# Optimization experiments

Measured on AMD Instinct MI355X. Metric: run time of the kernel, lower is better.

## Reference

```python
import jax, jax.numpy as jnp
import numpy as np

DIM = 64
HID = 128
DT_MAX = 0.1
BATCH = 16384


def _lin_init(k, fi, fo):
    kw, kb = jax.random.split(k)
    s = 1.0 / np.sqrt(fi)
    w = jax.random.uniform(kw, (fi, fo), minval=-s, maxval=s, dtype=jnp.float32)
    b = jax.random.uniform(kb, (fo,), minval=-s, maxval=s, dtype=jnp.float32)
    return w, b


def setup_inputs() -> dict:
    key = jax.random.key(0)
    ks = list(jax.random.split(key, 16))
    it = iter(ks)
    inp = {"z": jax.random.normal(next(it), (BATCH, DIM), dtype=jnp.float32)}
    layouts = [
        ("H", [(DIM, HID), (HID, HID), (HID, 1)]),
        ("D", [(DIM, HID), (HID, HID), (HID, 1)]),
        ("J", [(DIM, HID), (HID, DIM * DIM)]),
        ("B", [(DIM, HID), (HID, DIM * DIM)]),
        ("u", [(DIM, HID), (HID, DIM)]),
    ]
    for name, dims in layouts:
        for li, (fi, fo) in enumerate(dims, 1):
            w, b = _lin_init(next(it), fi, fo)
            inp[f"{name}w{li}"] = w
            inp[f"{name}b{li}"] = b
    inp["dt_logit"] = jnp.zeros((), dtype=jnp.float32)
    inp["energy_target"] = jnp.asarray(1.0, dtype=jnp.float32)
    return inp


def _scalar_net(z, w1, b1, w2, b2, w3, b3):
    # Linear->SiLU->Linear->SiLU->Linear, then softplus, squeeze -> [B]
    h = jax.nn.silu(z @ w1 + b1)
    h = jax.nn.silu(h @ w2 + b2)
    return jax.nn.softplus((h @ w3 + b3)[..., 0])


def reference(z, Hw1, Hb1, Hw2, Hb2, Hw3, Hb3,
              Dw1, Db1, Dw2, Db2, Dw3, Db3,
              Jw1, Jb1, Jw2, Jb2, Bw1, Bb1, Bw2, Bb2,
              uw1, ub1, uw2, ub2, dt_logit, energy_target):
    H = _scalar_net(z, Hw1, Hb1, Hw2, Hb2, Hw3, Hb3)  # [B]
    # autograd.grad(H.sum(), z) / grad(D.sum(), z)
    gH = jax.grad(lambda zz: _scalar_net(zz, Hw1, Hb1, Hw2, Hb2, Hw3, Hb3).sum())(z)
    gD = jax.grad(lambda zz: _scalar_net(zz, Dw1, Db1, Dw2, Db2, Dw3, Db3).sum())(z)
    # skew-symmetric J
    A = (jax.nn.silu(z @ Jw1 + Jb1) @ Jw2 + Jb2).reshape(-1, DIM, DIM)
    Jm = A - jnp.swapaxes(A, 1, 2)
    # PSD R = B B^T
    Bm = (jax.nn.silu(z @ Bw1 + Bb1) @ Bw2 + Bb2).reshape(-1, DIM, DIM)
    R = jnp.einsum('bik,bjk->bij', Bm, Bm)
    cons = jnp.einsum('bij,bj->bi', Jm, gH)
    diss = -jnp.einsum('bij,bj->bi', R, gD)
    u = jnp.tanh(z @ uw1 + ub1) @ uw2 + ub2
    pump = (energy_target - H)[:, None] * u
    dt = jax.nn.sigmoid(dt_logit) * DT_MAX
    dz = cons + diss + 0.1 * pump
    return z + dt * dz
```

## Files before the change

kernel.cpp:

```cpp
#include <hip/hip_runtime.h>

#define DIM 64
#define HID 128

typedef __attribute__((ext_vector_type(8))) short short8;
typedef __attribute__((ext_vector_type(4))) float f32x4;
typedef _Float16 h16x8 __attribute__((ext_vector_type(8)));
typedef _Float16 h16x2 __attribute__((ext_vector_type(2)));
typedef unsigned short ushort_t;

#define MFMA(A, B, C) __builtin_amdgcn_mfma_f32_16x16x32_bf16((A), (B), (C), 0, 0, 0)
#define MFMAH(A, B, C) __builtin_amdgcn_mfma_f32_16x16x32_f16((A), (B), (C), 0, 0, 0)
#define GLOAD_LDS(gp, lp) __builtin_amdgcn_global_load_lds( \
    (const __attribute__((address_space(1))) void*)(gp),    \
    (__attribute__((address_space(3))) void*)(lp), 16, 0, 0)

__device__ __forceinline__ float sigm(float x) { return 1.f / (1.f + __expf(-x)); }
__device__ __forceinline__ float siluf(float x) { return x * sigm(x); }
__device__ __forceinline__ float silup(float x) { float s = sigm(x); return s + x * s * (1.f - s); }
__device__ __forceinline__ float softplusf(float x) {
    if (x > 20.f) return x;
    return log1pf(__expf(x));
}
__device__ __forceinline__ ushort_t f2bf(float f) {
    union { float f; unsigned int u; } v; v.f = f;
    unsigned int r = v.u + 0x7fffu + ((v.u >> 16) & 1u);
    return (ushort_t)(r >> 16);
}
__device__ __forceinline__ ushort_t f2h(float f) {
    _Float16 h = (_Float16)f;
    union { _Float16 h; ushort_t u; } v; v.h = h; return v.u;
}
__device__ __forceinline__ _Float16 u2h(ushort_t u) {
    union { ushort_t u; _Float16 h; } v; v.u = u; return v.h;
}

#define OFF_HW1F  0
#define OFF_HW2F  8192
#define OFF_HW2TF 24576
#define OFF_HW1TF 40960
#define OFF_DW1F  49152
#define OFF_DW2F  57344
#define OFF_DW2TF 73728
#define OFF_DW1TF 90112
#define OFF_UW1F  98304
#define OFF_UW2F  106496
#define OFF_JW1F  114688
#define OFF_BW1F  122880

extern "C" __global__ __launch_bounds__(256)
void prep3_kernel(const float* __restrict__ Jw2, const float* __restrict__ Jb2,
                  const float* __restrict__ Bw2, const float* __restrict__ Bb2,
                  const float* __restrict__ Hw1, const float* __restrict__ Hw2,
                  const float* __restrict__ Dw1, const float* __restrict__ Dw2,
                  const float* __restrict__ uw1, const float* __restrict__ uw2,
                  const float* __restrict__ Jw1, const float* __restrict__ Bw1,
                  ushort_t* __restrict__ JW, ushort_t* __restrict__ BW1, ushort_t* __restrict__ BW2,
                  ushort_t* __restrict__ JbdF, ushort_t* __restrict__ Bb2F, ushort_t* __restrict__ Bb2TF,
                  ushort_t* __restrict__ SWF)
{
    const int b = blockIdx.x;
    if (b < 6144) {
        const int m = b >> 11;
        const int o = ((b & 2047) << 8) | threadIdx.x;
        const int e = o & 7, n = (o >> 3) & 63, g = (o >> 9) & 3, kt = o >> 11;
        const int k = (kt << 5) | (g << 3) | e;
        const int oi = k >> 7, h = k & 127;
        float val;
        if (m == 0)      val = Jw2[h * 4096 + n * 64 + oi] - Jw2[h * 4096 + oi * 64 + n];
        else if (m == 1) val = Bw2[h * 4096 + oi * 64 + n];
        else             val = Bw2[h * 4096 + n * 64 + oi];
        ushort_t* dst = (m == 0) ? JW : (m == 1) ? BW1 : BW2;
        dst[o] = f2h(val);
    } else if (b == 6144) {
        for (int e0 = threadIdx.x; e0 < 12288; e0 += 256) {
            const int m = e0 >> 12, o = e0 & 4095;
            const int e = o & 7, n = (o >> 3) & 63, g = (o >> 9) & 3, kb = o >> 11;
            const int k = (kb << 5) | (g << 3) | e;
            float val; ushort_t* dst;
            if (m == 0)      { val = Jb2[n * 64 + k] - Jb2[k * 64 + n]; dst = JbdF; }
            else if (m == 1) { val = Bb2[k * 64 + n];                   dst = Bb2F; }
            else             { val = Bb2[n * 64 + k];                   dst = Bb2TF; }
            dst[o] = f2h(val);
        }
    } else {
        const int e = (b - 6145) * 256 + threadIdx.x;
        float val = 0.f;
        if (e < 98304) {
            const int net = e / 49152;
            const int o = e - net * 49152;
            const float* W1s = net ? Dw1 : Hw1;
            const float* W2s = net ? Dw2 : Hw2;
            if (o < 8192) {
                int ks = o & 31, n = (o >> 5) & 127, kt = o >> 12;
                val = W1s[(kt * 32 + ks) * 128 + n];
            } else if (o < 24576) {
                int o2 = o - 8192;
                int ks = o2 & 31, n = (o2 >> 5) & 127, kt = o2 >> 12;
                val = W2s[(kt * 32 + ks) * 128 + n];
            } else if (o < 40960) {
                int o3 = o - 24576;
                int ks = o3 & 31, n = (o3 >> 5) & 127, kt = o3 >> 12;
                val = W2s[n * 128 + kt * 32 + ks];
            } else {
                int o4 = o - 40960;
                int ks = o4 & 31, n = (o4 >> 5) & 63, kt = o4 >> 11;
                val = W1s[n * 128 + kt * 32 + ks];
            }
        } else if (e < 106496) {
            int o = e - 98304;
            int ks = o & 31, n = (o >> 5) & 127, kt = o >> 12;
            val = uw1[(kt * 32 + ks) * 128 + n];
        } else if (e < 114688) {
            int o = e - 106496;
            int ks = o & 31, n = (o >> 5) & 63, kt = o >> 11;
            val = uw2[(kt * 32 + ks) * 64 + n];
        } else if (e < 122880) {
            int o = e - 114688;
            int ks = o & 31, n = (o >> 5) & 127, kt = o >> 12;
            val = Jw1[(kt * 32 + ks) * 128 + n];
        } else {
            int o = e - 122880;
            int ks = o & 31, n = (o >> 5) & 127, kt = o >> 12;
            val = Bw1[(kt * 32 + ks) * 128 + n];
        }
        SWF[e] = f2bf(val);
    }
}

__device__ __forceinline__ void scalar_net(
    int tid, int r0,
    const ushort_t* zbp, ushort_t* S1, ushort_t* S2, ushort_t* S3,
    float* yacc, float* srow, float* Hrow,
    const ushort_t* W1f, const ushort_t* W2f, const ushort_t* W2Tf, const ushort_t* W1Tf,
    const float* B1, const float* B2, const float* W3, const float* B3,
    ushort_t* gOut, int storeH)
{
    const int lane = tid & 63, w = tid >> 6;
    const int mt = w & 1, nh = w >> 1;
    const int cl = lane & 15, qq = lane >> 4;
    const int arow = mt * 16 + cl;
    const int crow = mt * 16 + qq * 4;

    {
        short8 a0 = *(const short8*)&zbp[arow * 72 + (qq << 3)];
        short8 a1 = *(const short8*)&zbp[arow * 72 + 32 + (qq << 3)];
        #pragma unroll
        for (int nt = 0; nt < 2; ++nt) {
            int n = nh * 32 + nt * 16 + cl;
            f32x4 acc = {0.f, 0.f, 0.f, 0.f};
            short8 b0 = *(const short8*)&W1f[(n << 5) + (qq << 3)];
            short8 b1 = *(const short8*)&W1f[((128 + n) << 5) + (qq << 3)];
            acc = MFMA(a0, b0, acc); acc = MFMA(a1, b1, acc);
            float bv = B1[n];
            #pragma unroll
            for (int q = 0; q < 4; ++q) {
                float aa = acc[q] + bv;
                S1[(crow + q) * 136 + n] = f2bf(siluf(aa));
                S2[(crow + q) * 136 + n] = f2bf(silup(aa));
            }
        }
    }
    __syncthreads();
    {
        short8 a[4];
        #pragma unroll
        for (int kt = 0; kt < 4; ++kt)
            a[kt] = *(const short8*)&S1[arow * 136 + kt * 32 + (qq << 3)];
        float yp[4] = {0.f, 0.f, 0.f, 0.f};
        #pragma unroll
        for (int nt = 0; nt < 2; ++nt) {
            int n = nh * 32 + nt * 16 + cl;
            f32x4 acc = {0.f, 0.f, 0.f, 0.f};
            #pragma unroll
            for (int kt = 0; kt < 4; ++kt) {
                short8 bb = *(const short8*)&W2f[((kt * 128 + n) << 5) + (qq << 3)];
                acc = MFMA(a[kt], bb, acc);
            }
            float bv = B2[n], w3v = W3[n];
            #pragma unroll
            for (int q = 0; q < 4; ++q) {
                float a2 = acc[q] + bv;
                yp[q] += siluf(a2) * w3v;
                S3[(crow + q) * 136 + n] = f2bf(w3v * silup(a2));
            }
        }
        #pragma unroll
        for (int q = 0; q < 4; ++q) {
            float p = yp[q];
            p += __shfl_xor(p, 1); p += __shfl_xor(p, 2);
            p += __shfl_xor(p, 4); p += __shfl_xor(p, 8);
            if (cl == 0) atomicAdd(&yacc[crow + q], p);
        }
    }
    __syncthreads();
    if (tid < 32) {
        float a3 = yacc[tid] + B3[0];
        srow[tid] = sigm(a3);
        if (storeH) Hrow[tid] = softplusf(a3);
        yacc[tid] = 0.f;
    }
    __syncthreads();
    {
        short8 a[4];
        #pragma unroll
        for (int kt = 0; kt < 4; ++kt)
            a[kt] = *(const short8*)&S3[arow * 136 + kt * 32 + (qq << 3)];
        #pragma unroll
        for (int nt = 0; nt < 2; ++nt) {
            int n = nh * 32 + nt * 16 + cl;
            f32x4 acc = {0.f, 0.f, 0.f, 0.f};
            #pragma unroll
            for (int kt = 0; kt < 4; ++kt) {
                short8 bb = *(const short8*)&W2Tf[((kt * 128 + n) << 5) + (qq << 3)];
                acc = MFMA(a[kt], bb, acc);
            }
            #pragma unroll
            for (int q = 0; q < 4; ++q) {
                float sp;
                { union { unsigned int u; float f; } v;
                  v.u = ((unsigned int)S2[(crow + q) * 136 + n]) << 16; sp = v.f; }
                S1[(crow + q) * 136 + n] = f2bf(acc[q] * sp);
            }
        }
    }
    __syncthreads();
    {
        short8 a[4];
        #pragma unroll
        for (int kt = 0; kt < 4; ++kt)
            a[kt] = *(const short8*)&S1[arow * 136 + kt * 32 + (qq << 3)];
        int n = nh * 16 + cl;
        f32x4 acc = {0.f, 0.f, 0.f, 0.f};
        #pragma unroll
        for (int kt = 0; kt < 4; ++kt) {
            short8 bb = *(const short8*)&W1Tf[((kt * 64 + n) << 5) + (qq << 3)];
            acc = MFMA(a[kt], bb, acc);
        }
        #pragma unroll
        for (int q = 0; q < 4; ++q) {
            int row = crow + q;
            gOut[(size_t)(r0 + row) * 64 + n] = f2h(srow[row] * acc[q]);
        }
    }
    __syncthreads();
}

extern "C" __global__ __launch_bounds__(512, 4)
void k1_kernel(const float* __restrict__ z,
               const float* __restrict__ Hb1, const float* __restrict__ Hb2,
               const float* __restrict__ Hw3, const float* __restrict__ Hb3,
               const float* __restrict__ Db1, const float* __restrict__ Db2,
               const float* __restrict__ Dw3, const float* __restrict__ Db3,
               const float* __restrict__ ub1, const float* __restrict__ ub2,
               const float* __restrict__ dtl, const float* __restrict__ etg,
               const ushort_t* __restrict__ SWF,
               ushort_t* __restrict__ gHbf, ushort_t* __restrict__ gDbf,
               float* __restrict__ out)
{
    __shared__ __align__(16) ushort_t zb[32][72];
    __shared__ __align__(16) ushort_t S1[32][136];
    __shared__ __align__(16) ushort_t S2[32][136];
    __shared__ __align__(16) ushort_t S3[32][136];
    __shared__ float yacc[32];
    __shared__ float srow[32];
    __shared__ float Hrow[32];

    const int tid = threadIdx.x;
    const int r0 = blockIdx.x * 32;

    {
        const float4* zg = (const float4*)(z + (size_t)r0 * 64);
        float4 v = zg[tid];
        int row = tid >> 4, c4 = (tid & 15) * 4;
        zb[row][c4 + 0] = f2bf(v.x); zb[row][c4 + 1] = f2bf(v.y);
        zb[row][c4 + 2] = f2bf(v.z); zb[row][c4 + 3] = f2bf(v.w);
        if (tid < 32) yacc[tid] = 0.f;
    }
    __syncthreads();

    scalar_net(tid, r0, &zb[0][0], &S1[0][0], &S2[0][0], &S3[0][0], yacc, srow, Hrow,
               SWF + OFF_HW1F, SWF + OFF_HW2F, SWF + OFF_HW2TF, SWF + OFF_HW1TF,
               Hb1, Hb2, Hw3, Hb3, gHbf, 1);
    scalar_net(tid, r0, &zb[0][0], &S1[0][0], &S2[0][0], &S3[0][0], yacc, srow, Hrow,
               SWF + OFF_DW1F, SWF + OFF_DW2F, SWF + OFF_DW2TF, SWF + OFF_DW1TF,
               Db1, Db2, Dw3, Db3, gDbf, 0);

    const int lane = tid & 63, w = tid >> 6;
    const int mt = w & 1, nh = w >> 1;
    const int cl = lane & 15, qq = lane >> 4;
    const int arow = mt * 16 + cl;
    const int crow = mt * 16 + qq * 4;

    {
        short8 a0 = *(const short8*)&zb[arow][(qq << 3)];
        short8 a1 = *(const short8*)&zb[arow][32 + (qq << 3)];
        const ushort_t* W1f = SWF + OFF_UW1F;
        #pragma unroll
        for (int nt = 0; nt < 2; ++nt) {
            int n = nh * 32 + nt * 16 + cl;
            f32x4 acc = {0.f, 0.f, 0.f, 0.f};
            short8 b0 = *(const short8*)&W1f[(n << 5) + (qq << 3)];
            short8 b1 = *(const short8*)&W1f[((128 + n) << 5) + (qq << 3)];
            acc = MFMA(a0, b0, acc); acc = MFMA(a1, b1, acc);
            float bv = ub1[n];
            #pragma unroll
            for (int q = 0; q < 4; ++q)
                S1[crow + q][n] = f2bf(tanhf(acc[q] + bv));
        }
    }
    __syncthreads();
    {
        short8 a[4];
        #pragma unroll
        for (int kt = 0; kt < 4; ++kt)
            a[kt] = *(const short8*)&S1[arow][kt * 32 + (qq << 3)];
        const ushort_t* W2f = SWF + OFF_UW2F;
        const float dtv = 0.1f * sigm(dtl[0]);
        const float et = etg[0];
        int n = nh * 16 + cl;
        f32x4 acc = {0.f, 0.f, 0.f, 0.f};
        #pragma unroll
        for (int kt = 0; kt < 4; ++kt) {
            short8 bb = *(const short8*)&W2f[((kt * 64 + n) << 5) + (qq << 3)];
            acc = MFMA(a[kt], bb, acc);
        }
        float bv = ub2[n];
        #pragma unroll
        for (int q = 0; q < 4; ++q) {
            int row = crow + q;
            size_t idx = (size_t)(r0 + row) * 64 + n;
            out[idx] = z[idx] + dtv * 0.1f * (et - Hrow[row]) * (acc[q] + bv);
        }
    }
}

#define LOADHF2H(SRC, HA, HB)                                                     \
    do {                                                                          \
        _Pragma("unroll")                                                         \
        for (int q4 = 0; q4 < 4; ++q4) {                                          \
            short8 sa = *(const short8*)&(SRC)[rr0][q4 * 32 + (qq << 3)];         \
            short8 sb = *(const short8*)&(SRC)[rr1][q4 * 32 + (qq << 3)];         \
            _Pragma("unroll")                                                     \
            for (int e = 0; e < 4; ++e) {                                         \
                h16x2 ta, tb;                                                     \
                ta[0] = u2h((ushort_t)sa[e * 2]); ta[1] = u2h((ushort_t)sa[e * 2 + 1]); \
                tb[0] = u2h((ushort_t)sb[e * 2]); tb[1] = u2h((ushort_t)sb[e * 2 + 1]); \
                (HA)[q4 * 4 + e] = ta;                                            \
                (HB)[q4 * 4 + e] = tb;                                            \
            }                                                                     \
        }                                                                         \
    } while (0)

#define STAGE(dst, src)                                                           \
    do {                                                                          \
        _Pragma("unroll")                                                         \
        for (int i_ = 0; i_ < 8; ++i_) {                                          \
            GLOAD_LDS((src) + ((w * 8 + i_) << 9) + (lane << 3),                  \
                      (dst) + ((w * 8 + i_) << 9));                               \
        }                                                                         \
    } while (0)

#define HEAVY_PASS(Wbase, BFbase, G, HA, HB, A00, A01, A10, A11)                  \
    do {                                                                          \
        STAGE(wst0, (Wbase));                                                     \
        __syncthreads();                                                          \
        _Pragma("unroll 1")                                                       \
        for (int t = 0; t < 32; ++t) {                                            \
            const ushort_t* curb = (t & 1) ? wst1 : wst0;                         \
            if (t < 31) STAGE((t & 1) ? wst0 : wst1, (Wbase) + (size_t)(t + 1) * 16384); \
            const int j = 2 * t + ks;                                             \
            _Float16 gA = u2h((G)[rr0][j]);                                       \
            _Float16 gB = u2h((G)[rr1][j]);                                       \
            h16x2 gA2; gA2[0] = gA; gA2[1] = gA;                                  \
            h16x2 gB2; gB2[0] = gB; gB2[1] = gB;                                  \
            _Pragma("unroll")                                                     \
            for (int ki = 0; ki < 4; ++ki) {                                      \
                const int tb = ((ks * 4 + ki) << 11) + (qq << 9);                 \
                h16x8 b0 = *(const h16x8*)&curb[tb + col0 * 8];                   \
                h16x8 b1 = *(const h16x8*)&curb[tb + col1 * 8];                   \
                union { h16x2 h2[4]; h16x8 v; } aA, aB;                           \
                _Pragma("unroll")                                                 \
                for (int e = 0; e < 4; ++e) {                                     \
                    aA.h2[e] = (HA)[ki * 4 + e] * gA2;                            \
                    aB.h2[e] = (HB)[ki * 4 + e] * gB2;                            \
                }                                                                 \
                A00 = MFMAH(aA.v, b0, A00); A01 = MFMAH(aA.v, b1, A01);           \
                A10 = MFMAH(aB.v, b0, A10); A11 = MFMAH(aB.v, b1, A11);           \
            }                                                                     \
            __syncthreads();                                                      \
        }                                                                         \
                             \
        {                                                                         \
            h16x8 abA = *(const h16x8*)&(G)[rr0][(ks << 5) + (qq << 3)];          \
            h16x8 abB = *(const h16x8*)&(G)[rr1][(ks << 5) + (qq << 3)];          \
            const ushort_t* bp = (BFbase) + (ks << 11) + (qq << 9);               \
            h16x8 b0 = *(const h16x8*)&bp[col0 * 8];                              \
            h16x8 b1 = *(const h16x8*)&bp[col1 * 8];                              \
            A00 = MFMAH(abA, b0, A00); A01 = MFMAH(abA, b1, A01);                 \
            A10 = MFMAH(abB, b0, A10); A11 = MFMAH(abB, b1, A11);                 \
        }                                                                         \
                                             \
        __syncthreads();                                                          \
        if (ks == 1) {                                                            \
            _Pragma("unroll")                                                     \
            for (int q = 0; q < 4; ++q) {                                         \
                Pb[orow0 + q][col0] = A00[q]; Pb[orow0 + q][col1] = A01[q];       \
                Pb[orow1 + q][col0] = A10[q]; Pb[orow1 + q][col1] = A11[q];       \
            }                                                                     \
        }                                                                         \
        __syncthreads();                                                          \
        if (ks == 0) {                                                            \
            _Pragma("unroll")                                                     \
            for (int q = 0; q < 4; ++q) {                                         \
                A00[q] += Pb[orow0 + q][col0]; A01[q] += Pb[orow0 + q][col1];     \
                A10[q] += Pb[orow1 + q][col0]; A11[q] += Pb[orow1 + q][col1];     \
            }                                                                     \
        }                                                                         \
        __syncthreads();                                                          \
    } while (0)

extern "C" __global__ __launch_bounds__(256, 2)
void k2_kernel(const float* __restrict__ z,
               const float* __restrict__ Jb1, const float* __restrict__ Bb1,
               const float* __restrict__ dtl,
               const ushort_t* __restrict__ JW, const ushort_t* __restrict__ BW1,
               const ushort_t* __restrict__ BW2,
               const ushort_t* __restrict__ JbdF, const ushort_t* __restrict__ Bb2F,
               const ushort_t* __restrict__ Bb2TF,
               const ushort_t* __restrict__ SWF,
               const ushort_t* __restrict__ gHbf, const ushort_t* __restrict__ gDbf,
               float* __restrict__ out)
{
    __shared__ __align__(16) ushort_t zb[32][72];
    __shared__ __align__(16) ushort_t hJ2[32][136];
    __shared__ __align__(16) ushort_t hB2[32][136];
    __shared__ __align__(16) ushort_t gHb[32][72];
    __shared__ __align__(16) ushort_t gDb[32][72];
    __shared__ __align__(16) ushort_t vb2[32][72];
    __shared__ __align__(16) float Pb[32][68];
    __shared__ __align__(16) ushort_t wst0[8192];
    __shared__ __align__(16) ushort_t wst1[8192];

    const int tid = threadIdx.x;
    const int r0 = blockIdx.x * 32;

    {
        const float4* zg = (const float4*)(z + (size_t)r0 * 64);
        #pragma unroll
        for (int it = 0; it < 2; ++it) {
            int i = it * 256 + tid;
            float4 v = zg[i];
            int row = i >> 4, c4 = (i & 15) * 4;
            zb[row][c4 + 0] = f2bf(v.x); zb[row][c4 + 1] = f2bf(v.y);
            zb[row][c4 + 2] = f2bf(v.z); zb[row][c4 + 3] = f2bf(v.w);
        }
        const short8* gh = (const short8*)(gHbf + (size_t)r0 * 64);
        const short8* gd = (const short8*)(gDbf + (size_t)r0 * 64);
        int row = tid >> 3, s = tid & 7;
        *(short8*)&gHb[row][s * 8] = gh[tid];
        *(short8*)&gDb[row][s * 8] = gd[tid];
    }
    __syncthreads();

    const int lane = tid & 63, w = tid >> 6;
    const int cl = lane & 15, qq = lane >> 4;
    const int mt = w & 1, nh = w >> 1;
    const int arow = mt * 16 + cl;
    const int crowL = mt * 16 + qq * 4;

    {
        short8 a0 = *(const short8*)&zb[arow][(qq << 3)];
        short8 a1 = *(const short8*)&zb[arow][32 + (qq << 3)];
        const ushort_t* JW1f = SWF + OFF_JW1F;
        const ushort_t* BW1f = SWF + OFF_BW1F;
        #pragma unroll
        for (int nt = 0; nt < 4; ++nt) {
            int n = nh * 64 + nt * 16 + cl;
            f32x4 accJ = {0.f, 0.f, 0.f, 0.f}, accB = {0.f, 0.f, 0.f, 0.f};
            short8 jb0 = *(const short8*)&JW1f[(n << 5) + (qq << 3)];
            short8 jb1 = *(const short8*)&JW1f[((128 + n) << 5) + (qq << 3)];
            accJ = MFMA(a0, jb0, accJ); accJ = MFMA(a1, jb1, accJ);
            short8 bb0 = *(const short8*)&BW1f[(n << 5) + (qq << 3)];
            short8 bb1 = *(const short8*)&BW1f[((128 + n) << 5) + (qq << 3)];
            accB = MFMA(a0, bb0, accB); accB = MFMA(a1, bb1, accB);
            float jbv = Jb1[n], bbv = Bb1[n];
            #pragma unroll
            for (int q = 0; q < 4; ++q) {
                hJ2[crowL + q][n] = f2h(siluf(accJ[q] + jbv));
                hB2[crowL + q][n] = f2h(siluf(accB[q] + bbv));
            }
        }
    }
    __syncthreads();

    const int ch = w & 1;
    const int ks = w >> 1;
    const int rr0 = cl;
    const int rr1 = cl + 16;
    const int col0 = ch * 32 + cl;
    const int col1 = col0 + 16;
    const int orow0 = qq * 4;
    const int orow1 = orow0 + 16;

    h16x2 hfJA[16], hfJB[16], hfBA[16], hfBB[16];
    f32x4 c00 = {0,0,0,0}, c01 = {0,0,0,0}, c10 = {0,0,0,0}, c11 = {0,0,0,0};
    f32x4 v00 = {0,0,0,0}, v01 = {0,0,0,0}, v10 = {0,0,0,0}, v11 = {0,0,0,0};
    f32x4 d00 = {0,0,0,0}, d01 = {0,0,0,0}, d10 = {0,0,0,0}, d11 = {0,0,0,0};

    LOADHF2H(hJ2, hfJA, hfJB);
    HEAVY_PASS(JW, JbdF, gHb, hfJA, hfJB, c00, c01, c10, c11);

    LOADHF2H(hB2, hfBA, hfBB);
    HEAVY_PASS(BW1, Bb2F, gDb, hfBA, hfBB, v00, v01, v10, v11);

    if (ks == 0) {
        #pragma unroll
        for (int q = 0; q < 4; ++q) {
            vb2[orow0 + q][col0] = f2h(v00[q]); vb2[orow0 + q][col1] = f2h(v01[q]);
            vb2[orow1 + q][col0] = f2h(v10[q]); vb2[orow1 + q][col1] = f2h(v11[q]);
        }
    }
    __syncthreads();

    HEAVY_PASS(BW2, Bb2TF, vb2, hfBA, hfBB, d00, d01, d10, d11);

    if (ks == 0) {
        const float dtv = 0.1f * sigm(dtl[0]);
        #pragma unroll
        for (int q = 0; q < 4; ++q) {
            size_t i00 = (size_t)(r0 + orow0 + q) * 64 + col0;
            size_t i01 = (size_t)(r0 + orow0 + q) * 64 + col1;
            size_t i10 = (size_t)(r0 + orow1 + q) * 64 + col0;
            size_t i11 = (size_t)(r0 + orow1 + q) * 64 + col1;
            out[i00] += dtv * (c00[q] - d00[q]);
            out[i01] += dtv * (c01[q] - d01[q]);
            out[i10] += dtv * (c10[q] - d10[q]);
            out[i11] += dtv * (c11[q] - d11[q]);
        }
    }
}

extern "C" void kernel_launch(void* const* d_in, const int* in_sizes, int n_in,
                              void* d_out, int out_size, void* d_ws, size_t ws_size,
                              hipStream_t stream) {
    const float* p[27];
    for (int i = 0; i < 27; ++i) p[i] = (const float*)d_in[i];
    ushort_t* JW    = (ushort_t*)d_ws;
    ushort_t* BW1   = JW + 524288;
    ushort_t* BW2   = BW1 + 524288;
    ushort_t* JbdF  = BW2 + 524288;
    ushort_t* Bb2F  = JbdF + 4096;
    ushort_t* Bb2TF = Bb2F + 4096;
    ushort_t* gHbf  = Bb2TF + 4096;
    ushort_t* gDbf  = gHbf + (size_t)16384 * 64;
    ushort_t* SWF   = gDbf + (size_t)16384 * 64;

    hipLaunchKernelGGL(prep3_kernel, dim3(6657), dim3(256), 0, stream,
                       p[15], p[16], p[19], p[20],
                       p[1], p[3], p[7], p[9],
                       p[21], p[23], p[13], p[17],
                       JW, BW1, BW2, JbdF, Bb2F, Bb2TF, SWF);

    const int batch = in_sizes[0] / DIM;
    hipLaunchKernelGGL(k1_kernel, dim3(batch / 32), dim3(512), 0, stream,
                       p[0],
                       p[2], p[4], p[5], p[6],
                       p[8], p[10], p[11], p[12],
                       p[22], p[24],
                       p[25], p[26],
                       SWF, gHbf, gDbf, (float*)d_out);

    hipLaunchKernelGGL(k2_kernel, dim3(batch / 32), dim3(256), 0, stream,
                       p[0], p[14], p[18], p[25],
                       JW, BW1, BW2, JbdF, Bb2F, Bb2TF, SWF,
                       gHbf, gDbf, (float*)d_out);
}
```

Baseline: 119.5 us.

## Load heavy-pass weight fragments directly from global memory instead of LDS staging

Replaces the double-buffered global-to-LDS staging of the large weight tiles in the heavy pass with direct per-lane global loads into registers, unrolled by two. This removes the per-iteration __syncthreads barriers and frees 32 KB of shared memory, which may allow more blocks per CU. In exchange, each wave fetches its weight fragments straight from global/L2 with no LDS-level sharing across waves, and load latency must be hidden by unrolling and occupancy.

New measurement: 112.5 us. -5.9%, faster.

```diff
diff --git a/kernel.cpp b/kernel.cpp
--- a/kernel.cpp
+++ b/kernel.cpp
@@ -11,9 +11,6 @@
 
 #define MFMA(A, B, C) __builtin_amdgcn_mfma_f32_16x16x32_bf16((A), (B), (C), 0, 0, 0)
 #define MFMAH(A, B, C) __builtin_amdgcn_mfma_f32_16x16x32_f16((A), (B), (C), 0, 0, 0)
-#define GLOAD_LDS(gp, lp) __builtin_amdgcn_global_load_lds( \
-    (const __attribute__((address_space(1))) void*)(gp),    \
-    (__attribute__((address_space(3))) void*)(lp), 16, 0, 0)
 
 __device__ __forceinline__ float sigm(float x) { return 1.f / (1.f + __expf(-x)); }
 __device__ __forceinline__ float siluf(float x) { return x * sigm(x); }
@@ -352,51 +349,41 @@
         }                                                                         \
     } while (0)
 
-#define STAGE(dst, src)                                                           \
-    do {                                                                          \
-        _Pragma("unroll")                                                         \
-        for (int i_ = 0; i_ < 8; ++i_) {                                          \
-            GLOAD_LDS((src) + ((w * 8 + i_) << 9) + (lane << 3),                  \
-                      (dst) + ((w * 8 + i_) << 9));                               \
-        }                                                                         \
-    } while (0)
-
 #define HEAVY_PASS(Wbase, BFbase, G, HA, HB, A00, A01, A10, A11)                  \
     do {                                                                          \
-        STAGE(wst0, (Wbase));                                                     \
-        __syncthreads();                                                          \
-        _Pragma("unroll 1")                                                       \
-        for (int t = 0; t < 32; ++t) {                                            \
-            const ushort_t* curb = (t & 1) ? wst1 : wst0;                         \
-            if (t < 31) STAGE((t & 1) ? wst0 : wst1, (Wbase) + (size_t)(t + 1) * 16384); \
-            const int j = 2 * t + ks;                                             \
+        _Pragma("unroll 2")                                                       \
+        for (int jj = 0; jj < 32; ++jj) {                                         \
+            const int j = 2 * jj + ks;                                            \
+            const ushort_t* bp = (Wbase) + (size_t)j * 8192 + (qq << 9);          \
+            h16x8 bf0[4], bf1[4];                                                 \
+            _Pragma("unroll")                                                     \
+            for (int ki = 0; ki < 4; ++ki) {                                      \
+                bf0[ki] = *(const h16x8*)&bp[ki * 2048 + col0 * 8];               \
+                bf1[ki] = *(const h16x8*)&bp[ki * 2048 + col1 * 8];               \
+            }                                                                     \
             _Float16 gA = u2h((G)[rr0][j]);                                       \
             _Float16 gB = u2h((G)[rr1][j]);                                       \
             h16x2 gA2; gA2[0] = gA; gA2[1] = gA;                                  \
             h16x2 gB2; gB2[0] = gB; gB2[1] = gB;                                  \
             _Pragma("unroll")                                                     \
             for (int ki = 0; ki < 4; ++ki) {                                      \
-                const int tb = ((ks * 4 + ki) << 11) + (qq << 9);                 \
-                h16x8 b0 = *(const h16x8*)&curb[tb + col0 * 8];                   \
-                h16x8 b1 = *(const h16x8*)&curb[tb + col1 * 8];                   \
                 union { h16x2 h2[4]; h16x8 v; } aA, aB;                           \
                 _Pragma("unroll")                                                 \
                 for (int e = 0; e < 4; ++e) {                                     \
                     aA.h2[e] = (HA)[ki * 4 + e] * gA2;                            \
                     aB.h2[e] = (HB)[ki * 4 + e] * gB2;                            \
                 }                                                                 \
-                A00 = MFMAH(aA.v, b0, A00); A01 = MFMAH(aA.v, b1, A01);           \
-                A10 = MFMAH(aB.v, b0, A10); A11 = MFMAH(aB.v, b1, A11);           \
+                A00 = MFMAH(aA.v, bf0[ki], A00); A01 = MFMAH(aA.v, bf1[ki], A01); \
+                A10 = MFMAH(aB.v, bf0[ki], A10); A11 = MFMAH(aB.v, bf1[ki], A11); \
             }                                                                     \
-            __syncthreads();                                                      \
         }                                                                         \
                              \
         {                                                                         \
             h16x8 abA = *(const h16x8*)&(G)[rr0][(ks << 5) + (qq << 3)];          \
             h16x8 abB = *(const h16x8*)&(G)[rr1][(ks << 5) + (qq << 3)];          \
-            const ushort_t* bp = (BFbase) + (ks << 11) + (qq << 9);               \
-            h16x8 b0 = *(const h16x8*)&bp[col0 * 8];                              \
-            h16x8 b1 = *(const h16x8*)&bp[col1 * 8];                              \
+            const ushort_t* bpb = (BFbase) + (ks << 11) + (qq << 9);              \
+            h16x8 b0 = *(const h16x8*)&bpb[col0 * 8];                             \
+            h16x8 b1 = *(const h16x8*)&bpb[col1 * 8];                             \
             A00 = MFMAH(abA, b0, A00); A01 = MFMAH(abA, b1, A01);                 \
             A10 = MFMAH(abB, b0, A10); A11 = MFMAH(abB, b1, A11);                 \
         }                                                                         \
@@ -439,8 +426,6 @@
     __shared__ __align__(16) ushort_t gDb[32][72];
     __shared__ __align__(16) ushort_t vb2[32][72];
     __shared__ __align__(16) float Pb[32][68];
-    __shared__ __align__(16) ushort_t wst0[8192];
-    __shared__ __align__(16) ushort_t wst1[8192];
 
     const int tid = threadIdx.x;
     const int r0 = blockIdx.x * 32;
```
